# Kernel optimization log

Hardware: AMD Instinct MI355X
Metric: run time of the kernel (lower is better)

## Reference

```python
import jax, jax.numpy as jnp
import numpy as np

B = 2097152
IND = 10
DIM = 32
L = 4
M = DIM // 2 + 1  # 17 rfft bins
EPS = 1e-5


def setup_inputs() -> dict:
    key = jax.random.key(0)
    ks = jax.random.split(key, 16)
    scale = 1.0 / (DIM * DIM)
    inp = {
        'x': jax.random.normal(ks[0], (B, IND), dtype=jnp.float32),
        # stem / head Linear weights stored as [in, out] (x @ W + b)
        'stem_w': jax.random.normal(ks[1], (IND, DIM), jnp.float32) * (1.0 / np.sqrt(IND)),
        'stem_b': jnp.zeros((DIM,), jnp.float32),
        # Fourier weights: torch.rand complex -> real & imag ~ U[0,1), scaled
        'fno_wr': scale * jax.random.uniform(ks[2], (L, M, M), jnp.float32),
        'fno_wi': scale * jax.random.uniform(ks[3], (L, M, M), jnp.float32),
        # ResidualBlock params, stacked over layers
        'bn1_g': jnp.ones((L, DIM), jnp.float32),
        'bn1_b': jnp.zeros((L, DIM), jnp.float32),
        'lin1_w': jax.random.normal(ks[4], (L, DIM, DIM), jnp.float32) * (1.0 / np.sqrt(DIM)),
        'lin1_b': jnp.zeros((L, DIM), jnp.float32),
        'bn2_g': jnp.ones((L, DIM), jnp.float32),
        'bn2_b': jnp.zeros((L, DIM), jnp.float32),
        'lin2_w': jax.random.normal(ks[5], (L, DIM, DIM), jnp.float32) * (1.0 / np.sqrt(DIM)),
        'lin2_b': jnp.zeros((L, DIM), jnp.float32),
        'head_w': jax.random.normal(ks[6], (DIM, IND), jnp.float32) * (1.0 / np.sqrt(DIM)),
        'head_b': jnp.zeros((IND,), jnp.float32),
    }
    return inp


def _bn(h, g, b):
    # BatchNorm1d in training mode: biased batch stats over the batch dim
    mu = jnp.mean(h, axis=0)
    var = jnp.mean(jnp.square(h - mu), axis=0)
    return (h - mu) * jax.lax.rsqrt(var + EPS) * g + b


def reference(x, stem_w, stem_b, fno_wr, fno_wi, bn1_g, bn1_b, lin1_w, lin1_b,
              bn2_g, bn2_b, lin2_w, lin2_b, head_w, head_b):
    h = x @ stem_w + stem_b  # [B, DIM]
    n_layers = fno_wr.shape[0]
    for i in range(n_layers):
        # FourierBlock: rfft -> complex channel mix -> irfft (bias=False)
        w = fno_wr[i] + 1j * fno_wi[i]  # [M, M] complex
        hf = jnp.fft.rfft(h, axis=-1)  # [B, M] complex
        x1 = jnp.fft.irfft(hf @ w, n=DIM, axis=-1)  # [B, DIM]
        # ResidualBlock: BN -> SiLU -> Linear -> BN -> SiLU -> Linear, + identity skip
        r = jax.nn.silu(_bn(h, bn1_g[i], bn1_b[i])) @ lin1_w[i] + lin1_b[i]
        r = jax.nn.silu(_bn(r, bn2_g[i], bn2_b[i])) @ lin2_w[i] + lin2_b[i]
        x2 = r + h
        h = jax.nn.silu(x1 + x2)
    return h @ head_w + head_b  # [B, IND]
```

## Files before the change

kernel.cpp:

```cpp
#include <hip/hip_runtime.h>
#include <math.h>

#define BATCH   2097152
#define NTILES  (BATCH / 16)
#define GRID    2048
#define BLOCK   256
#define WAVES   (GRID * (BLOCK / 64))
#define NREP    16
#define NSETS   8

typedef __attribute__((ext_vector_type(8))) short short8;
typedef __attribute__((ext_vector_type(4))) float f32x4;
typedef unsigned short ushort_t;

__device__ __forceinline__ int chan_of(int s) { return (s >> 1) + ((s & 1) << 4); }

__device__ __forceinline__ float silu_f(float x) {
    return x * __builtin_amdgcn_rcpf(1.0f + __expf(-x));
}
__device__ __forceinline__ unsigned cvt_pk_bf16(float lo, float hi) {
    unsigned r;
    asm("v_cvt_pk_bf16_f32 %0, %1, %2" : "=v"(r) : "v"(lo), "v"(hi));
    return r;
}
__device__ __forceinline__ unsigned short f2bf(float f) {
    union { float f; unsigned u; } v; v.f = f;
    unsigned r = v.u + 0x7fffu + ((v.u >> 16) & 1u);
    return (unsigned short)(r >> 16);
}
__device__ __forceinline__ float bf2f(unsigned short b) {
    union { unsigned u; float f; } v; v.u = ((unsigned)b) << 16;
    return v.f;
}
__device__ __forceinline__ short8 pack8(const float* f) {
    union { short8 s; unsigned u[4]; } r;
    #pragma unroll
    for (int i = 0; i < 4; ++i) r.u[i] = cvt_pk_bf16(f[2 * i], f[2 * i + 1]);
    return r.s;
}
__device__ __forceinline__ f32x4 mfma16(short8 a, short8 b, f32x4 c) {
    return __builtin_amdgcn_mfma_f32_16x16x32_bf16(a, b, c, 0, 0, 0);
}
__device__ __forceinline__ short8 wfrag(const float* W, int ldN, int K, int lane, int half, int N) {
    short8 r;
    const int n = (lane & 15) + 16 * half;
    const int k0 = (lane >> 4) * 8;
    #pragma unroll
    for (int j = 0; j < 8; ++j) {
        const int ck = chan_of(k0 + j);
        const float v = (ck < K && n < N) ? W[ck * ldN + n] : 0.f;
        ((unsigned short*)&r)[j] = f2bf(v);
    }
    return r;
}
__device__ __forceinline__ void bn_coef(const double* sIn, const float* g, const float* b,
                                        int c, float* A, float* C) {
    double s = 0, q = 0;
    #pragma unroll
    for (int r = 0; r < NREP; ++r) { s += sIn[r * 64 + c]; q += sIn[r * 64 + 32 + c]; }
    const double inv = 1.0 / (double)BATCH;
    const double mu = s * inv, var = q * inv - mu * mu;
    const float a = (float)(1.0 / sqrt(var + 1e-5)) * g[c];
    *A = a; *C = b[c] - (float)mu * a;
}
__device__ __forceinline__ void stats_reduce_c(float sS0, float sQ0, float sS1, float sQ1,
                                               float (*sRed)[64], double* sOut, int tid) {
    const int lane = tid & 63, wid = tid >> 6;
    sS0 += __shfl_down(sS0, 32); sS0 += __shfl_down(sS0, 16);
    sQ0 += __shfl_down(sQ0, 32); sQ0 += __shfl_down(sQ0, 16);
    sS1 += __shfl_down(sS1, 32); sS1 += __shfl_down(sS1, 16);
    sQ1 += __shfl_down(sQ1, 32); sQ1 += __shfl_down(sQ1, 16);
    if (lane < 16) {
        sRed[wid][lane] = sS0; sRed[wid][16 + lane] = sS1;
        sRed[wid][32 + lane] = sQ0; sRed[wid][48 + lane] = sQ1;
    }
    __syncthreads();
    if (tid < 64) {
        const float tot = sRed[0][tid] + sRed[1][tid] + sRed[2][tid] + sRed[3][tid];
        atomicAdd(sOut + tid, (double)tot);
    }
}

__global__ void setup_f_kernel(const float* __restrict__ wr, const float* __restrict__ wi,
                               float* __restrict__ Fp)
{
    __shared__ double cs[32], sn[32];
    const int l = blockIdx.x, tid = threadIdx.x;
    if (tid < 32) {
        double a = (2.0 * 3.14159265358979323846 / 32.0) * (double)tid;
        cs[tid] = cos(a); sn[tid] = sin(a);
    }
    __syncthreads();
    const float* wrl = wr + l * 289;
    const float* wil = wi + l * 289;
    for (int p = tid; p < 1024; p += BLOCK) {
        const int d = p >> 5, j = p & 31;
        double acc = 0.0;
        for (int m = 0; m < 17; ++m) {
            double yr = 0.0, yi = 0.0;
            for (int k = 0; k < 17; ++k) {
                const double c = cs[(k * d) & 31], s = sn[(k * d) & 31];
                const double a = (double)wrl[k * 17 + m], b = (double)wil[k * 17 + m];
                yr += c * a + s * b;
                yi += c * b - s * a;
            }
            const double alpha = (m == 0 || m == 16) ? 1.0 : 2.0;
            acc += alpha * (cs[(j * m) & 31] * yr - sn[(j * m) & 31] * yi);
        }
        const double F = acc * (1.0 / 32.0);
        Fp[l * 1024 + d * 32 + j] = (float)(F + ((d == j) ? 1.0 : 0.0));
    }
}

__global__ __launch_bounds__(BLOCK) void stem_kernel(
    const float* __restrict__ x, const float* __restrict__ sw, const float* __restrict__ sb,
    ushort_t* __restrict__ h, double* __restrict__ sOut)
{
    __shared__ ushort_t tile[4][512] __attribute__((aligned(16)));
    __shared__ float sRed[4][64];
    const int tid = threadIdx.x, lane = tid & 63, wid = tid >> 6;
    const int m = lane & 15, q = lane >> 4;
    const short8 B0 = wfrag(sw, 32, 10, lane, 0, 32);
    const short8 B1 = wfrag(sw, 32, 10, lane, 1, 32);
    const float bc0 = sb[m], bc1 = sb[m + 16];
    float sS0 = 0, sQ0 = 0, sS1 = 0, sQ1 = 0;
    ushort_t* myT = tile[wid];
    for (int t = blockIdx.x * (BLOCK / 64) + wid; t < NTILES; t += WAVES) {
        const size_t rb = (size_t)t * 16;
        float c4[4];
        #pragma unroll
        for (int i2 = 0; i2 < 2; ++i2) {
            const int k = q * 4 + 2 * i2;
            if (k + 1 < 10) {
                const float2 v = *(const float2*)(x + (rb + m) * 10 + k);
                c4[2 * i2] = v.x; c4[2 * i2 + 1] = v.y;
            } else { c4[2 * i2] = 0.f; c4[2 * i2 + 1] = 0.f; }
        }
        float xv[8];
        #pragma unroll
        for (int j = 0; j < 8; ++j) xv[j] = (j & 1) ? 0.f : c4[j >> 1];
        const short8 xa = pack8(xv);
        f32x4 a0 = {bc0, bc0, bc0, bc0}, a1 = {bc1, bc1, bc1, bc1};
        a0 = mfma16(xa, B0, a0);
        a1 = mfma16(xa, B1, a1);
        #pragma unroll
        for (int r = 0; r < 4; ++r) {
            sS0 += a0[r]; sQ0 += a0[r] * a0[r];
            sS1 += a1[r]; sQ1 += a1[r] * a1[r];
        }
        __builtin_amdgcn_wave_barrier();
        #pragma unroll
        for (int r = 0; r < 4; ++r)
            *(unsigned*)&myT[(q * 4 + r) * 32 + 2 * m] = cvt_pk_bf16(a0[r], a1[r]);
        __builtin_amdgcn_wave_barrier();
        const short8 hv = *(const short8*)(myT + lane * 8);
        *(short8*)(h + rb * 32 + lane * 8) = hv;
        __builtin_amdgcn_wave_barrier();
    }
    stats_reduce_c(sS0, sQ0, sS1, sQ1, sRed, sOut + (size_t)(blockIdx.x & (NREP - 1)) * 64, tid);
}

__global__ __launch_bounds__(BLOCK) void p1_kernel(
    const ushort_t* __restrict__ h_in, const double* __restrict__ sIn, double* __restrict__ sOut,
    const float* __restrict__ g1, const float* __restrict__ b1,
    const float* __restrict__ w1, const float* __restrict__ lb1)
{
    __shared__ float cA[32], cC[32];
    __shared__ float sRed[4][64];
    const int tid = threadIdx.x, lane = tid & 63, wid = tid >> 6;
    if (tid < 32) bn_coef(sIn, g1, b1, tid, &cA[tid], &cC[tid]);
    __syncthreads();
    const int m = lane & 15, q = lane >> 4;
    float a1k[8], c1k[8];
    #pragma unroll
    for (int j = 0; j < 8; ++j) {
        const int c = chan_of(q * 8 + j);
        a1k[j] = cA[c]; c1k[j] = cC[c];
    }
    const short8 W10 = wfrag(w1, 32, 32, lane, 0, 32);
    const short8 W11 = wfrag(w1, 32, 32, lane, 1, 32);
    const float lbc0 = lb1[m], lbc1 = lb1[m + 16];
    float sS0 = 0, sQ0 = 0, sS1 = 0, sQ1 = 0;
    for (int t = blockIdx.x * (BLOCK / 64) + wid; t < NTILES; t += WAVES) {
        const size_t rb = (size_t)t * 16;
        const short8 ha = *(const short8*)(h_in + (rb + m) * 32 + q * 8);
        float tf[8];
        #pragma unroll
        for (int j = 0; j < 8; ++j)
            tf[j] = silu_f(a1k[j] * bf2f(((const unsigned short*)&ha)[j]) + c1k[j]);
        const short8 ta = pack8(tf);
        f32x4 r0 = {lbc0, lbc0, lbc0, lbc0}, r1 = {lbc1, lbc1, lbc1, lbc1};
        r0 = mfma16(ta, W10, r0);
        r1 = mfma16(ta, W11, r1);
        #pragma unroll
        for (int r = 0; r < 4; ++r) {
            sS0 += r0[r]; sQ0 += r0[r] * r0[r];
            sS1 += r1[r]; sQ1 += r1[r] * r1[r];
        }
    }
    stats_reduce_c(sS0, sQ0, sS1, sQ1, sRed, sOut + (size_t)(blockIdx.x & (NREP - 1)) * 64, tid);
}

template<bool LAST>
__global__ __launch_bounds__(BLOCK) void p2_kernel(
    const ushort_t* __restrict__ h_in, ushort_t* __restrict__ h_out, float* __restrict__ out,
    const double* __restrict__ sIn1, const double* __restrict__ sIn2, double* __restrict__ sOut,
    const float* __restrict__ g1, const float* __restrict__ b1,
    const float* __restrict__ w1, const float* __restrict__ lb1,
    const float* __restrict__ g2, const float* __restrict__ b2,
    const float* __restrict__ w2, const float* __restrict__ lb2,
    const float* __restrict__ Fp, const float* __restrict__ hw, const float* __restrict__ hb)
{
    __shared__ float cA1[32], cC1[32], cA2[32], cD2[32];
    __shared__ ushort_t tile[4][512] __attribute__((aligned(16)));
    __shared__ float sRed[4][64];
    const int tid = threadIdx.x, lane = tid & 63, wid = tid >> 6;
    if (tid < 32) {
        bn_coef(sIn1, g1, b1, tid, &cA1[tid], &cC1[tid]);
    } else if (tid < 64) {
        const int c = tid - 32;
        float A, C;
        bn_coef(sIn2, g2, b2, c, &A, &C);
        cA2[c] = A; cD2[c] = C + A * lb1[c];
    }
    __syncthreads();
    const int m = lane & 15, q = lane >> 4;
    float a1k[8], c1k[8];
    #pragma unroll
    for (int j = 0; j < 8; ++j) {
        const int c = chan_of(q * 8 + j);
        a1k[j] = cA1[c]; c1k[j] = cC1[c];
    }
    const float a2c0 = cA2[m], d2c0 = cD2[m], a2c1 = cA2[m + 16], d2c1 = cD2[m + 16];
    const float b2c0 = lb2[m], b2c1 = lb2[m + 16];
    const short8 W10 = wfrag(w1, 32, 32, lane, 0, 32);
    const short8 W11 = wfrag(w1, 32, 32, lane, 1, 32);
    const short8 W20 = wfrag(w2, 32, 32, lane, 0, 32);
    const short8 W21 = wfrag(w2, 32, 32, lane, 1, 32);
    const short8 F0  = wfrag(Fp, 32, 32, lane, 0, 32);
    const short8 F1  = wfrag(Fp, 32, 32, lane, 1, 32);
    short8 HW = {};
    float hbc = 0.f;
    if (LAST) { HW = wfrag(hw, 10, 32, lane, 0, 10); hbc = (m < 10) ? hb[m] : 0.f; }
    float sS0 = 0, sQ0 = 0, sS1 = 0, sQ1 = 0;
    ushort_t* myT = tile[wid];

    for (int t = blockIdx.x * (BLOCK / 64) + wid; t < NTILES; t += WAVES) {
        const size_t rb = (size_t)t * 16;
        const short8 ha = *(const short8*)(h_in + (rb + m) * 32 + q * 8);
        float tf[8];
        #pragma unroll
        for (int j = 0; j < 8; ++j)
            tf[j] = silu_f(a1k[j] * bf2f(((const unsigned short*)&ha)[j]) + c1k[j]);
        const short8 ta = pack8(tf);
        const f32x4 z = {0.f, 0.f, 0.f, 0.f};
        f32x4 r0 = mfma16(ta, W10, z);
        f32x4 r1 = mfma16(ta, W11, z);
        float uf0[4], uf1[4];
        #pragma unroll
        for (int r = 0; r < 4; ++r) {
            uf0[r] = silu_f(a2c0 * r0[r] + d2c0);
            uf1[r] = silu_f(a2c1 * r1[r] + d2c1);
        }
        __builtin_amdgcn_wave_barrier();
        #pragma unroll
        for (int r = 0; r < 4; ++r)
            *(unsigned*)&myT[(q * 4 + r) * 32 + 2 * m] = cvt_pk_bf16(uf0[r], uf1[r]);
        __builtin_amdgcn_wave_barrier();
        const short8 ua = *(const short8*)(myT + m * 32 + q * 8);
        f32x4 c0 = {b2c0, b2c0, b2c0, b2c0}, c1 = {b2c1, b2c1, b2c1, b2c1};
        c0 = mfma16(ha, F0, c0);  c1 = mfma16(ha, F1, c1);
        c0 = mfma16(ua, W20, c0); c1 = mfma16(ua, W21, c1);
        float hn0[4], hn1[4];
        #pragma unroll
        for (int r = 0; r < 4; ++r) { hn0[r] = silu_f(c0[r]); hn1[r] = silu_f(c1[r]); }
        __builtin_amdgcn_wave_barrier();
        #pragma unroll
        for (int r = 0; r < 4; ++r)
            *(unsigned*)&myT[(q * 4 + r) * 32 + 2 * m] = cvt_pk_bf16(hn0[r], hn1[r]);
        __builtin_amdgcn_wave_barrier();
        if (!LAST) {
            #pragma unroll
            for (int r = 0; r < 4; ++r) {
                sS0 += hn0[r]; sQ0 += hn0[r] * hn0[r];
                sS1 += hn1[r]; sQ1 += hn1[r] * hn1[r];
            }
            const short8 hv = *(const short8*)(myT + lane * 8);
            *(short8*)(h_out + rb * 32 + lane * 8) = hv;
        } else {
            const short8 hna = *(const short8*)(myT + m * 32 + q * 8);
            f32x4 oc = {hbc, hbc, hbc, hbc};
            oc = mfma16(hna, HW, oc);
            if (m < 10) {
                #pragma unroll
                for (int r = 0; r < 4; ++r) out[(rb + q * 4 + r) * 10 + m] = oc[r];
            }
        }
        __builtin_amdgcn_wave_barrier();
    }
    if (!LAST)
        stats_reduce_c(sS0, sQ0, sS1, sQ1, sRed, sOut + (size_t)(blockIdx.x & (NREP - 1)) * 64, tid);
}

extern "C" void kernel_launch(void* const* d_in, const int* in_sizes, int n_in,
                              void* d_out, int out_size, void* d_ws, size_t ws_size,
                              hipStream_t stream)
{
    const float* x      = (const float*)d_in[0];
    const float* stem_w = (const float*)d_in[1];
    const float* stem_b = (const float*)d_in[2];
    const float* fno_wr = (const float*)d_in[3];
    const float* fno_wi = (const float*)d_in[4];
    const float* bn1_g  = (const float*)d_in[5];
    const float* bn1_b  = (const float*)d_in[6];
    const float* lin1_w = (const float*)d_in[7];
    const float* lin1_b = (const float*)d_in[8];
    const float* bn2_g  = (const float*)d_in[9];
    const float* bn2_b  = (const float*)d_in[10];
    const float* lin2_w = (const float*)d_in[11];
    const float* lin2_b = (const float*)d_in[12];
    const float* head_w = (const float*)d_in[13];
    const float* head_b = (const float*)d_in[14];

    ushort_t* h  = (ushort_t*)d_ws;
    float*    Fp = (float*)((char*)d_ws + (size_t)BATCH * 32 * sizeof(ushort_t));
    double*   st = (double*)((char*)d_ws + (size_t)BATCH * 32 * sizeof(ushort_t) + 16384);

    hipMemsetAsync(st, 0, (size_t)NSETS * NREP * 64 * sizeof(double), stream);
    setup_f_kernel<<<4, BLOCK, 0, stream>>>(fno_wr, fno_wi, Fp);
    stem_kernel<<<GRID, BLOCK, 0, stream>>>(x, stem_w, stem_b, h, st);

    for (int l = 0; l < 4; ++l) {
        double* sH = st + (size_t)(2 * l) * NREP * 64;
        double* sR = st + (size_t)(2 * l + 1) * NREP * 64;
        p1_kernel<<<GRID, BLOCK, 0, stream>>>(
            h, sH, sR,
            bn1_g + l * 32, bn1_b + l * 32, lin1_w + l * 1024, lin1_b + l * 32);
        if (l < 3) {
            double* sN = st + (size_t)(2 * l + 2) * NREP * 64;
            p2_kernel<false><<<GRID, BLOCK, 0, stream>>>(
                h, h, nullptr, sH, sR, sN,
                bn1_g + l * 32, bn1_b + l * 32, lin1_w + l * 1024, lin1_b + l * 32,
                bn2_g + l * 32, bn2_b + l * 32, lin2_w + l * 1024, lin2_b + l * 32,
                Fp + l * 1024, nullptr, nullptr);
        } else {
            p2_kernel<true><<<GRID, BLOCK, 0, stream>>>(
                h, nullptr, (float*)d_out, sH, sR, st,
                bn1_g + l * 32, bn1_b + l * 32, lin1_w + l * 1024, lin1_b + l * 32,
                bn2_g + l * 32, bn2_b + l * 32, lin2_w + l * 1024, lin2_b + l * 32,
                Fp + l * 1024, head_w, head_b);
        }
    }
}
```

Measured before the change: 633.0 us.

## Store residual-branch activations in p1 and load them in p2 instead of recomputing

When the workspace is large enough, p1 now writes the first residual linear output (bf16) to a second buffer. A new p2 variant loads that buffer, applies only BN2, SiLU, lin2 and the Fourier mix, and no longer recomputes BN1, SiLU and lin1 from h. This trades redundant ALU and MFMA work for an extra bf16 activation-sized write in p1 and read in p2 each layer. The original recompute path is kept as a fallback for small workspaces.

```diff
diff --git a/kernel.cpp b/kernel.cpp
--- a/kernel.cpp
+++ b/kernel.cpp
@@ -160,12 +160,15 @@
     stats_reduce_c(sS0, sQ0, sS1, sQ1, sRed, sOut + (size_t)(blockIdx.x & (NREP - 1)) * 64, tid);
 }
 
+template<bool STORE_R>
 __global__ __launch_bounds__(BLOCK) void p1_kernel(
-    const ushort_t* __restrict__ h_in, const double* __restrict__ sIn, double* __restrict__ sOut,
+    const ushort_t* __restrict__ h_in, ushort_t* __restrict__ r_out,
+    const double* __restrict__ sIn, double* __restrict__ sOut,
     const float* __restrict__ g1, const float* __restrict__ b1,
     const float* __restrict__ w1, const float* __restrict__ lb1)
 {
     __shared__ float cA[32], cC[32];
+    __shared__ ushort_t tile[4][512] __attribute__((aligned(16)));
     __shared__ float sRed[4][64];
     const int tid = threadIdx.x, lane = tid & 63, wid = tid >> 6;
     if (tid < 32) bn_coef(sIn, g1, b1, tid, &cA[tid], &cC[tid]);
@@ -181,6 +184,7 @@
     const short8 W11 = wfrag(w1, 32, 32, lane, 1, 32);
     const float lbc0 = lb1[m], lbc1 = lb1[m + 16];
     float sS0 = 0, sQ0 = 0, sS1 = 0, sQ1 = 0;
+    ushort_t* myT = tile[wid];
     for (int t = blockIdx.x * (BLOCK / 64) + wid; t < NTILES; t += WAVES) {
         const size_t rb = (size_t)t * 16;
         const short8 ha = *(const short8*)(h_in + (rb + m) * 32 + q * 8);
@@ -197,12 +201,98 @@
             sS0 += r0[r]; sQ0 += r0[r] * r0[r];
             sS1 += r1[r]; sQ1 += r1[r] * r1[r];
         }
+        if (STORE_R) {
+            __builtin_amdgcn_wave_barrier();
+            #pragma unroll
+            for (int r = 0; r < 4; ++r)
+                *(unsigned*)&myT[(q * 4 + r) * 32 + 2 * m] = cvt_pk_bf16(r0[r], r1[r]);
+            __builtin_amdgcn_wave_barrier();
+            const short8 rv = *(const short8*)(myT + lane * 8);
+            *(short8*)(r_out + rb * 32 + lane * 8) = rv;
+            __builtin_amdgcn_wave_barrier();
+        }
     }
     stats_reduce_c(sS0, sQ0, sS1, sQ1, sRed, sOut + (size_t)(blockIdx.x & (NREP - 1)) * 64, tid);
 }
 
 template<bool LAST>
-__global__ __launch_bounds__(BLOCK) void p2_kernel(
+__global__ __launch_bounds__(BLOCK) void p2_kernel_ld(
+    const ushort_t* __restrict__ h_in, const ushort_t* __restrict__ r_in,
+    ushort_t* __restrict__ h_out, float* __restrict__ out,
+    const double* __restrict__ sIn2, double* __restrict__ sOut,
+    const float* __restrict__ g2, const float* __restrict__ b2,
+    const float* __restrict__ w2, const float* __restrict__ lb2,
+    const float* __restrict__ Fp, const float* __restrict__ hw, const float* __restrict__ hb)
+{
+    __shared__ float cA2[32], cC2[32];
+    __shared__ ushort_t tile[4][512] __attribute__((aligned(16)));
+    __shared__ float sRed[4][64];
+    const int tid = threadIdx.x, lane = tid & 63, wid = tid >> 6;
+    if (tid < 32) bn_coef(sIn2, g2, b2, tid, &cA2[tid], &cC2[tid]);
+    __syncthreads();
+    const int m = lane & 15, q = lane >> 4;
+    float a2k[8], c2k[8];
+    #pragma unroll
+    for (int j = 0; j < 8; ++j) {
+        const int c = chan_of(q * 8 + j);
+        a2k[j] = cA2[c]; c2k[j] = cC2[c];
+    }
+    const float b2c0 = lb2[m], b2c1 = lb2[m + 16];
+    const short8 W20 = wfrag(w2, 32, 32, lane, 0, 32);
+    const short8 W21 = wfrag(w2, 32, 32, lane, 1, 32);
+    const short8 F0  = wfrag(Fp, 32, 32, lane, 0, 32);
+    const short8 F1  = wfrag(Fp, 32, 32, lane, 1, 32);
+    short8 HW = {};
+    float hbc = 0.f;
+    if (LAST) { HW = wfrag(hw, 10, 32, lane, 0, 10); hbc = (m < 10) ? hb[m] : 0.f; }
+    float sS0 = 0, sQ0 = 0, sS1 = 0, sQ1 = 0;
+    ushort_t* myT = tile[wid];
+
+    for (int t = blockIdx.x * (BLOCK / 64) + wid; t < NTILES; t += WAVES) {
+        const size_t rb = (size_t)t * 16;
+        const short8 ha = *(const short8*)(h_in + (rb + m) * 32 + q * 8);
+        const short8 ra = *(const short8*)(r_in + (rb + m) * 32 + q * 8);
+        float uf[8];
+        #pragma unroll
+        for (int j = 0; j < 8; ++j)
+            uf[j] = silu_f(a2k[j] * bf2f(((const unsigned short*)&ra)[j]) + c2k[j]);
+        const short8 ua = pack8(uf);
+        f32x4 c0 = {b2c0, b2c0, b2c0, b2c0}, c1 = {b2c1, b2c1, b2c1, b2c1};
+        c0 = mfma16(ha, F0, c0);  c1 = mfma16(ha, F1, c1);
+        c0 = mfma16(ua, W20, c0); c1 = mfma16(ua, W21, c1);
+        float hn0[4], hn1[4];
+        #pragma unroll
+        for (int r = 0; r < 4; ++r) { hn0[r] = silu_f(c0[r]); hn1[r] = silu_f(c1[r]); }
+        __builtin_amdgcn_wave_barrier();
+        #pragma unroll
+        for (int r = 0; r < 4; ++r)
+            *(unsigned*)&myT[(q * 4 + r) * 32 + 2 * m] = cvt_pk_bf16(hn0[r], hn1[r]);
+        __builtin_amdgcn_wave_barrier();
+        if (!LAST) {
+            #pragma unroll
+            for (int r = 0; r < 4; ++r) {
+                sS0 += hn0[r]; sQ0 += hn0[r] * hn0[r];
+                sS1 += hn1[r]; sQ1 += hn1[r] * hn1[r];
+            }
+            const short8 hv = *(const short8*)(myT + lane * 8);
+            *(short8*)(h_out + rb * 32 + lane * 8) = hv;
+        } else {
+            const short8 hna = *(const short8*)(myT + m * 32 + q * 8);
+            f32x4 oc = {hbc, hbc, hbc, hbc};
+            oc = mfma16(hna, HW, oc);
+            if (m < 10) {
+                #pragma unroll
+                for (int r = 0; r < 4; ++r) out[(rb + q * 4 + r) * 10 + m] = oc[r];
+            }
+        }
+        __builtin_amdgcn_wave_barrier();
+    }
+    if (!LAST)
+        stats_reduce_c(sS0, sQ0, sS1, sQ1, sRed, sOut + (size_t)(blockIdx.x & (NREP - 1)) * 64, tid);
+}
+
+template<bool LAST>
+__global__ __launch_bounds__(BLOCK) void p2_kernel_rc(
     const ushort_t* __restrict__ h_in, ushort_t* __restrict__ h_out, float* __restrict__ out,
     const double* __restrict__ sIn1, const double* __restrict__ sIn2, double* __restrict__ sOut,
     const float* __restrict__ g1, const float* __restrict__ b1,
@@ -322,9 +412,15 @@
     const float* head_w = (const float*)d_in[13];
     const float* head_b = (const float*)d_in[14];
 
+    const size_t HBYTES = (size_t)BATCH * 32 * sizeof(ushort_t);
+    const size_t TAIL   = 16384 + (size_t)NSETS * NREP * 64 * sizeof(double);
+    const bool   big    = ws_size >= 2 * HBYTES + TAIL;
+
     ushort_t* h  = (ushort_t*)d_ws;
-    float*    Fp = (float*)((char*)d_ws + (size_t)BATCH * 32 * sizeof(ushort_t));
-    double*   st = (double*)((char*)d_ws + (size_t)BATCH * 32 * sizeof(ushort_t) + 16384);
+    ushort_t* rw = big ? (ushort_t*)((char*)d_ws + HBYTES) : nullptr;
+    char*     tp = (char*)d_ws + (big ? 2 * HBYTES : HBYTES);
+    float*    Fp = (float*)tp;
+    double*   st = (double*)(tp + 16384);
 
     hipMemsetAsync(st, 0, (size_t)NSETS * NREP * 64 * sizeof(double), stream);
     setup_f_kernel<<<4, BLOCK, 0, stream>>>(fno_wr, fno_wi, Fp);
@@ -333,22 +429,40 @@
     for (int l = 0; l < 4; ++l) {
         double* sH = st + (size_t)(2 * l) * NREP * 64;
         double* sR = st + (size_t)(2 * l + 1) * NREP * 64;
-        p1_kernel<<<GRID, BLOCK, 0, stream>>>(
-            h, sH, sR,
-            bn1_g + l * 32, bn1_b + l * 32, lin1_w + l * 1024, lin1_b + l * 32);
-        if (l < 3) {
-            double* sN = st + (size_t)(2 * l + 2) * NREP * 64;
-            p2_kernel<false><<<GRID, BLOCK, 0, stream>>>(
-                h, h, nullptr, sH, sR, sN,
-                bn1_g + l * 32, bn1_b + l * 32, lin1_w + l * 1024, lin1_b + l * 32,
-                bn2_g + l * 32, bn2_b + l * 32, lin2_w + l * 1024, lin2_b + l * 32,
-                Fp + l * 1024, nullptr, nullptr);
+        if (big) {
+            p1_kernel<true><<<GRID, BLOCK, 0, stream>>>(
+                h, rw, sH, sR,
+                bn1_g + l * 32, bn1_b + l * 32, lin1_w + l * 1024, lin1_b + l * 32);
+            if (l < 3) {
+                double* sN = st + (size_t)(2 * l + 2) * NREP * 64;
+                p2_kernel_ld<false><<<GRID, BLOCK, 0, stream>>>(
+                    h, rw, h, nullptr, sR, sN,
+                    bn2_g + l * 32, bn2_b + l * 32, lin2_w + l * 1024, lin2_b + l * 32,
+                    Fp + l * 1024, nullptr, nullptr);
+            } else {
+                p2_kernel_ld<true><<<GRID, BLOCK, 0, stream>>>(
+                    h, rw, nullptr, (float*)d_out, sR, st,
+                    bn2_g + l * 32, bn2_b + l * 32, lin2_w + l * 1024, lin2_b + l * 32,
+                    Fp + l * 1024, head_w, head_b);
+            }
         } else {
-            p2_kernel<true><<<GRID, BLOCK, 0, stream>>>(
-                h, nullptr, (float*)d_out, sH, sR, st,
-                bn1_g + l * 32, bn1_b + l * 32, lin1_w + l * 1024, lin1_b + l * 32,
-                bn2_g + l * 32, bn2_b + l * 32, lin2_w + l * 1024, lin2_b + l * 32,
-                Fp + l * 1024, head_w, head_b);
-        }
-    }
-}
+            p1_kernel<false><<<GRID, BLOCK, 0, stream>>>(
+                h, nullptr, sH, sR,
+                bn1_g + l * 32, bn1_b + l * 32, lin1_w + l * 1024, lin1_b + l * 32);
+            if (l < 3) {
+                double* sN = st + (size_t)(2 * l + 2) * NREP * 64;
+                p2_kernel_rc<false><<<GRID, BLOCK, 0, stream>>>(
+                    h, h, nullptr, sH, sR, sN,
+                    bn1_g + l * 32, bn1_b + l * 32, lin1_w + l * 1024, lin1_b + l * 32,
+                    bn2_g + l * 32, bn2_b + l * 32, lin2_w + l * 1024, lin2_b + l * 32,
+                    Fp + l * 1024, nullptr, nullptr);
+            } else {
+                p2_kernel_rc<true><<<GRID, BLOCK, 0, stream>>>(
+                    h, nullptr, (float*)d_out, sH, sR, st,
+                    bn1_g + l * 32, bn1_b + l * 32, lin1_w + l * 1024, lin1_b + l * 32,
+                    bn2_g + l * 32, bn2_b + l * 32, lin2_w + l * 1024, lin2_b + l * 32,
+                    Fp + l * 1024, head_w, head_b);
+            }
+        }
+    }
+}
```

Result: slower. 722.3 us (+14.1%).

## Swap MFMA operand order to keep results in A-fragment layout, drop LDS transposes

Applied to the files above, without the earlier changes.

MFMA operands are swapped (weights as A, activations as B), so each lane's accumulator holds consecutive channels of one row. That output layout matches the next MFMA's input fragment, so the LDS staging tiles and wave barriers between the chained matmuls are removed, and h is written straight to global memory as packed bf16 pairs. Per-channel BN coefficients, biases and the statistics accumulators become per-lane arrays of four, reduced with a new shuffle-based routine. The cost is narrower 4-byte global stores instead of 16-byte coalesced ones, plus a few more registers.

```diff
diff --git a/kernel.cpp b/kernel.cpp
--- a/kernel.cpp
+++ b/kernel.cpp
@@ -73,6 +73,34 @@
     if (lane < 16) {
         sRed[wid][lane] = sS0; sRed[wid][16 + lane] = sS1;
         sRed[wid][32 + lane] = sQ0; sRed[wid][48 + lane] = sQ1;
+    }
+    __syncthreads();
+    if (tid < 64) {
+        const float tot = sRed[0][tid] + sRed[1][tid] + sRed[2][tid] + sRed[3][tid];
+        atomicAdd(sOut + tid, (double)tot);
+    }
+}
+__device__ __forceinline__ void stats_reduce_r(float* sLo, float* sQLo, float* sHi, float* sQHi,
+                                               float (*sRed)[64], double* sOut, int tid) {
+    const int lane = tid & 63, wid = tid >> 6, q = lane >> 4;
+    #pragma unroll
+    for (int r = 0; r < 4; ++r) {
+        #pragma unroll
+        for (int off = 8; off; off >>= 1) {
+            sLo[r]  += __shfl_down(sLo[r],  off);
+            sQLo[r] += __shfl_down(sQLo[r], off);
+            sHi[r]  += __shfl_down(sHi[r],  off);
+            sQHi[r] += __shfl_down(sQHi[r], off);
+        }
+    }
+    if ((lane & 15) == 0) {
+        #pragma unroll
+        for (int r = 0; r < 4; ++r) {
+            sRed[wid][q * 4 + r]      = sLo[r];
+            sRed[wid][16 + q * 4 + r] = sHi[r];
+            sRed[wid][32 + q * 4 + r] = sQLo[r];
+            sRed[wid][48 + q * 4 + r] = sQHi[r];
+        }
     }
     __syncthreads();
     if (tid < 64) {
@@ -116,15 +144,15 @@
     const float* __restrict__ x, const float* __restrict__ sw, const float* __restrict__ sb,
     ushort_t* __restrict__ h, double* __restrict__ sOut)
 {
-    __shared__ ushort_t tile[4][512] __attribute__((aligned(16)));
     __shared__ float sRed[4][64];
     const int tid = threadIdx.x, lane = tid & 63, wid = tid >> 6;
     const int m = lane & 15, q = lane >> 4;
     const short8 B0 = wfrag(sw, 32, 10, lane, 0, 32);
     const short8 B1 = wfrag(sw, 32, 10, lane, 1, 32);
-    const float bc0 = sb[m], bc1 = sb[m + 16];
-    float sS0 = 0, sQ0 = 0, sS1 = 0, sQ1 = 0;
-    ushort_t* myT = tile[wid];
+    float sblo[4], sbhi[4];
+    #pragma unroll
+    for (int r = 0; r < 4; ++r) { sblo[r] = sb[q * 4 + r]; sbhi[r] = sb[16 + q * 4 + r]; }
+    float sLo[4] = {0,0,0,0}, sQLo[4] = {0,0,0,0}, sHi[4] = {0,0,0,0}, sQHi[4] = {0,0,0,0};
     for (int t = blockIdx.x * (BLOCK / 64) + wid; t < NTILES; t += WAVES) {
         const size_t rb = (size_t)t * 16;
         float c4[4];
@@ -140,24 +168,19 @@
         #pragma unroll
         for (int j = 0; j < 8; ++j) xv[j] = (j & 1) ? 0.f : c4[j >> 1];
         const short8 xa = pack8(xv);
-        f32x4 a0 = {bc0, bc0, bc0, bc0}, a1 = {bc1, bc1, bc1, bc1};
-        a0 = mfma16(xa, B0, a0);
-        a1 = mfma16(xa, B1, a1);
+        f32x4 a0 = {sblo[0], sblo[1], sblo[2], sblo[3]};
+        f32x4 a1 = {sbhi[0], sbhi[1], sbhi[2], sbhi[3]};
+        a0 = mfma16(B0, xa, a0);
+        a1 = mfma16(B1, xa, a1);
         #pragma unroll
         for (int r = 0; r < 4; ++r) {
-            sS0 += a0[r]; sQ0 += a0[r] * a0[r];
-            sS1 += a1[r]; sQ1 += a1[r] * a1[r];
-        }
-        __builtin_amdgcn_wave_barrier();
-        #pragma unroll
-        for (int r = 0; r < 4; ++r)
-            *(unsigned*)&myT[(q * 4 + r) * 32 + 2 * m] = cvt_pk_bf16(a0[r], a1[r]);
-        __builtin_amdgcn_wave_barrier();
-        const short8 hv = *(const short8*)(myT + lane * 8);
-        *(short8*)(h + rb * 32 + lane * 8) = hv;
-        __builtin_amdgcn_wave_barrier();
-    }
-    stats_reduce_c(sS0, sQ0, sS1, sQ1, sRed, sOut + (size_t)(blockIdx.x & (NREP - 1)) * 64, tid);
+            sLo[r] += a0[r]; sQLo[r] += a0[r] * a0[r];
+            sHi[r] += a1[r]; sQHi[r] += a1[r] * a1[r];
+            const unsigned w = cvt_pk_bf16(a0[r], a1[r]);
+            *(unsigned*)(h + (rb + m) * 32 + (size_t)(q * 4 + r) * 2) = w;
+        }
+    }
+    stats_reduce_r(sLo, sQLo, sHi, sQHi, sRed, sOut + (size_t)(blockIdx.x & (NREP - 1)) * 64, tid);
 }
 
 __global__ __launch_bounds__(BLOCK) void p1_kernel(
@@ -212,7 +235,6 @@
     const float* __restrict__ Fp, const float* __restrict__ hw, const float* __restrict__ hb)
 {
     __shared__ float cA1[32], cC1[32], cA2[32], cD2[32];
-    __shared__ ushort_t tile[4][512] __attribute__((aligned(16)));
     __shared__ float sRed[4][64];
     const int tid = threadIdx.x, lane = tid & 63, wid = tid >> 6;
     if (tid < 32) {
@@ -231,8 +253,15 @@
         const int c = chan_of(q * 8 + j);
         a1k[j] = cA1[c]; c1k[j] = cC1[c];
     }
-    const float a2c0 = cA2[m], d2c0 = cD2[m], a2c1 = cA2[m + 16], d2c1 = cD2[m + 16];
-    const float b2c0 = lb2[m], b2c1 = lb2[m + 16];
+    float a2lo[4], d2lo[4], a2hi[4], d2hi[4], blo[4], bhi[4], hbl[4];
+    #pragma unroll
+    for (int r = 0; r < 4; ++r) {
+        const int c = q * 4 + r;
+        a2lo[r] = cA2[c];      d2lo[r] = cD2[c];
+        a2hi[r] = cA2[c + 16]; d2hi[r] = cD2[c + 16];
+        blo[r] = lb2[c];       bhi[r] = lb2[c + 16];
+        hbl[r] = (LAST && c < 10) ? hb[c] : 0.f;
+    }
     const short8 W10 = wfrag(w1, 32, 32, lane, 0, 32);
     const short8 W11 = wfrag(w1, 32, 32, lane, 1, 32);
     const short8 W20 = wfrag(w2, 32, 32, lane, 0, 32);
@@ -240,10 +269,8 @@
     const short8 F0  = wfrag(Fp, 32, 32, lane, 0, 32);
     const short8 F1  = wfrag(Fp, 32, 32, lane, 1, 32);
     short8 HW = {};
-    float hbc = 0.f;
-    if (LAST) { HW = wfrag(hw, 10, 32, lane, 0, 10); hbc = (m < 10) ? hb[m] : 0.f; }
-    float sS0 = 0, sQ0 = 0, sS1 = 0, sQ1 = 0;
-    ushort_t* myT = tile[wid];
+    if (LAST) HW = wfrag(hw, 10, 32, lane, 0, 10);
+    float sLo[4] = {0,0,0,0}, sQLo[4] = {0,0,0,0}, sHi[4] = {0,0,0,0}, sQHi[4] = {0,0,0,0};
 
     for (int t = blockIdx.x * (BLOCK / 64) + wid; t < NTILES; t += WAVES) {
         const size_t rb = (size_t)t * 16;
@@ -254,52 +281,46 @@
             tf[j] = silu_f(a1k[j] * bf2f(((const unsigned short*)&ha)[j]) + c1k[j]);
         const short8 ta = pack8(tf);
         const f32x4 z = {0.f, 0.f, 0.f, 0.f};
-        f32x4 r0 = mfma16(ta, W10, z);
-        f32x4 r1 = mfma16(ta, W11, z);
-        float uf0[4], uf1[4];
+        f32x4 r0 = mfma16(W10, ta, z);
+        f32x4 r1 = mfma16(W11, ta, z);
+        float ulo[4], uhi[4];
         #pragma unroll
         for (int r = 0; r < 4; ++r) {
-            uf0[r] = silu_f(a2c0 * r0[r] + d2c0);
-            uf1[r] = silu_f(a2c1 * r1[r] + d2c1);
-        }
-        __builtin_amdgcn_wave_barrier();
-        #pragma unroll
-        for (int r = 0; r < 4; ++r)
-            *(unsigned*)&myT[(q * 4 + r) * 32 + 2 * m] = cvt_pk_bf16(uf0[r], uf1[r]);
-        __builtin_amdgcn_wave_barrier();
-        const short8 ua = *(const short8*)(myT + m * 32 + q * 8);
-        f32x4 c0 = {b2c0, b2c0, b2c0, b2c0}, c1 = {b2c1, b2c1, b2c1, b2c1};
-        c0 = mfma16(ha, F0, c0);  c1 = mfma16(ha, F1, c1);
-        c0 = mfma16(ua, W20, c0); c1 = mfma16(ua, W21, c1);
-        float hn0[4], hn1[4];
-        #pragma unroll
-        for (int r = 0; r < 4; ++r) { hn0[r] = silu_f(c0[r]); hn1[r] = silu_f(c1[r]); }
-        __builtin_amdgcn_wave_barrier();
-        #pragma unroll
-        for (int r = 0; r < 4; ++r)
-            *(unsigned*)&myT[(q * 4 + r) * 32 + 2 * m] = cvt_pk_bf16(hn0[r], hn1[r]);
-        __builtin_amdgcn_wave_barrier();
+            ulo[r] = silu_f(a2lo[r] * r0[r] + d2lo[r]);
+            uhi[r] = silu_f(a2hi[r] * r1[r] + d2hi[r]);
+        }
+        union { short8 s; unsigned u[4]; } uau;
+        #pragma unroll
+        for (int i = 0; i < 4; ++i) uau.u[i] = cvt_pk_bf16(ulo[i], uhi[i]);
+        const short8 ua = uau.s;
+        f32x4 c0 = {blo[0], blo[1], blo[2], blo[3]};
+        f32x4 c1 = {bhi[0], bhi[1], bhi[2], bhi[3]};
+        c0 = mfma16(F0, ha, c0);  c1 = mfma16(F1, ha, c1);
+        c0 = mfma16(W20, ua, c0); c1 = mfma16(W21, ua, c1);
+        float hnlo[4], hnhi[4];
+        #pragma unroll
+        for (int r = 0; r < 4; ++r) { hnlo[r] = silu_f(c0[r]); hnhi[r] = silu_f(c1[r]); }
         if (!LAST) {
             #pragma unroll
             for (int r = 0; r < 4; ++r) {
-                sS0 += hn0[r]; sQ0 += hn0[r] * hn0[r];
-                sS1 += hn1[r]; sQ1 += hn1[r] * hn1[r];
+                sLo[r] += hnlo[r]; sQLo[r] += hnlo[r] * hnlo[r];
+                sHi[r] += hnhi[r]; sQHi[r] += hnhi[r] * hnhi[r];
+                const unsigned w = cvt_pk_bf16(hnlo[r], hnhi[r]);
+                *(unsigned*)(h_out + (rb + m) * 32 + (size_t)(q * 4 + r) * 2) = w;
             }
-            const short8 hv = *(const short8*)(myT + lane * 8);
-            *(short8*)(h_out + rb * 32 + lane * 8) = hv;
         } else {
-            const short8 hna = *(const short8*)(myT + m * 32 + q * 8);
-            f32x4 oc = {hbc, hbc, hbc, hbc};
-            oc = mfma16(hna, HW, oc);
-            if (m < 10) {
-                #pragma unroll
-                for (int r = 0; r < 4; ++r) out[(rb + q * 4 + r) * 10 + m] = oc[r];
-            }
-        }
-        __builtin_amdgcn_wave_barrier();
+            union { short8 s; unsigned u[4]; } hnu;
+            #pragma unroll
+            for (int i = 0; i < 4; ++i) hnu.u[i] = cvt_pk_bf16(hnlo[i], hnhi[i]);
+            f32x4 oc = {hbl[0], hbl[1], hbl[2], hbl[3]};
+            oc = mfma16(HW, hnu.s, oc);
+            #pragma unroll
+            for (int r = 0; r < 4; ++r)
+                if (q * 4 + r < 10) out[(rb + m) * 10 + q * 4 + r] = oc[r];
+        }
     }
     if (!LAST)
-        stats_reduce_c(sS0, sQ0, sS1, sQ1, sRed, sOut + (size_t)(blockIdx.x & (NREP - 1)) * 64, tid);
+        stats_reduce_r(sLo, sQLo, sHi, sQHi, sRed, sOut + (size_t)(blockIdx.x & (NREP - 1)) * 64, tid);
 }
 
 extern "C" void kernel_launch(void* const* d_in, const int* in_sizes, int n_in,
```

New measurement: 634.1 us. Within noise of the previous version (+0.2%).
